# Optimization experiments

Measured on AMD Instinct MI355X. Metric: run time of the kernel, lower is better.

Reference implementation:

```python
import jax, jax.numpy as jnp
import numpy as np

T, B, H = 2048, 32, 512

def setup_inputs() -> dict:
    key = jax.random.key(0)
    k1, k2, k3, k4 = jax.random.split(key, 4)
    hidden = jax.random.normal(k1, (1, B, H), dtype=jnp.float32)
    encoder_outputs = jax.random.normal(k2, (T, B, H), dtype=jnp.float32)
    # nn.Linear(2H, H): weight (H, 2H), bias (H,)
    bound = 1.0 / np.sqrt(2 * H)
    W_attn = jax.random.uniform(k3, (H, 2 * H), dtype=jnp.float32, minval=-bound, maxval=bound)
    b_attn = jax.random.uniform(jax.random.fold_in(k3, 1), (H,), dtype=jnp.float32, minval=-bound, maxval=bound)
    stdv = 1.0 / np.sqrt(H)
    v = jax.random.normal(k4, (H,), dtype=jnp.float32) * stdv
    return {"hidden": hidden, "encoder_outputs": encoder_outputs,
            "W_attn": W_attn, "b_attn": b_attn, "v": v}

def reference(hidden, encoder_outputs, W_attn, b_attn, v):
    # hidden: (1,B,H) -> broadcast to (B,T,H); enc: (T,B,H) -> (B,T,H)
    enc = jnp.transpose(encoder_outputs, (1, 0, 2))          # (B,T,H)
    h = jnp.broadcast_to(hidden[0][:, None, :], enc.shape)   # (B,T,H)
    cat = jnp.concatenate([h, enc], axis=2)                  # (B,T,2H)
    energy = jnp.tanh(jnp.einsum('bth,oh->bto', cat, W_attn) + b_attn)  # (B,T,H)
    scores = jnp.einsum('bth,h->bt', energy, v)              # (B,T)
    return jax.nn.softmax(scores, axis=1)[:, None, :]        # (B,1,T)
```

## Files before the change

kernel.cpp:

```cpp
#include <hip/hip_runtime.h>
#include <hip/hip_bf16.h>


#define TT 2048
#define BB 32
#define HH 512

typedef __attribute__((ext_vector_type(8))) short bf16x8;
typedef __attribute__((ext_vector_type(4))) float f32x4;

static __device__ __forceinline__ unsigned cvt2(float a, float b) {
    union { __hip_bfloat162 h; unsigned u; } cv;
    cv.h = __float22bfloat162_rn(make_float2(a, b));
    return cv.u;
}

static __device__ __forceinline__ unsigned short f2bf(float f) {
    unsigned int u = __float_as_uint(f);
    unsigned int r = (u + 0x7FFFu + ((u >> 16) & 1u)) >> 16;
    return (unsigned short)r;
}

static __device__ __forceinline__ float fast_tanh(float x) {
    float e = __expf(2.0f * x);
    return 1.0f - 2.0f * __builtin_amdgcn_rcpf(1.0f + e);
}

static __device__ __forceinline__ void gload_lds16(const void* g, void* l) {
    __builtin_amdgcn_global_load_lds(
        (const __attribute__((address_space(1))) unsigned int*)g,
        (__attribute__((address_space(3))) unsigned int*)l, 16, 0, 0);
}

__global__ void prep_kernel(const float* __restrict__ W,
                            const float* __restrict__ hidden,
                            const float* __restrict__ b_attn,
                            short* __restrict__ W2p,
                            float* __restrict__ hb) {
    __shared__ float hrow[512];
    const int bid = blockIdx.x;
    if (bid < 1024) {
        int idx = bid * 256 + threadIdx.x;
        int nt = idx >> 16;
        int ks = (idx >> 13) & 7;
        int s  = idx & 8191;
        int j  = s >> 6;
        int c  = s & 63;
        int o  = nt * 128 + j;
        int k  = ks * 64 + (c ^ ((j & 7) << 3));
        W2p[idx] = (short)f2bf(W[o * 1024 + 512 + k]);
    } else {
        const int hbid = bid - 1024;
        int b = hbid >> 1;
        int o = ((hbid & 1) << 8) + threadIdx.x;
        for (int h = threadIdx.x; h < 512; h += 256) hrow[h] = hidden[b * 512 + h];
        __syncthreads();
        const float4* wr = reinterpret_cast<const float4*>(W + (size_t)o * 1024);
        const float4* hr = reinterpret_cast<const float4*>(hrow);
        float acc = b_attn[o];
#pragma unroll 8
        for (int i = 0; i < 128; ++i) {
            float4 w = wr[i], h4 = hr[i];
            acc += w.x * h4.x + w.y * h4.y + w.z * h4.z + w.w * h4.w;
        }
        hb[b * 512 + o] = acc;
    }
}

__global__ __launch_bounds__(256, 2) void attn_main_kernel(
    const float* __restrict__ enc, const short* __restrict__ W2p,
    const float* __restrict__ hb, const float* __restrict__ v,
    float* __restrict__ scores_part)
{
    __shared__ short As[2][128 * 64];
    __shared__ short Bs[2][128 * 64];
    __shared__ float s_red[2][128];

    const int tid = threadIdx.x;
    const int bid = blockIdx.x;
    const int w = (bid & 7) * 256 + (bid >> 3);
    const int nt = w & 3;
    const int mtile = w >> 2;
    const int r0 = mtile * 128;

    const int wave = tid >> 6;
    const int lane = tid & 63;
    const int wr = wave >> 1;
    const int wc = wave & 1;
    const int lcol = lane & 15;
    const int lq = lane >> 4;

    const int arow = tid >> 3;
    const int afc = (tid & 7) * 8;
    const float* encbase = enc + (size_t)(r0 + arow) * HH + afc;
    const short* bsrc = W2p + nt * 65536 + (wave * 4) * 512 + lane * 8;

    f32x4 acc[4][4];
#pragma unroll
    for (int mt = 0; mt < 4; ++mt)
#pragma unroll
        for (int ns = 0; ns < 4; ++ns) acc[mt][ns] = (f32x4){0.f, 0.f, 0.f, 0.f};

    float4 rA0[8], rA1[8];

#define A_LOAD(RA, KS)                                                              \
    {                                                                               \
        _Pragma("unroll")                                                           \
        for (int p = 0; p < 4; ++p) {                                               \
            const float* src = encbase + (size_t)p * 32 * HH + (KS) * 64;           \
            RA[p * 2]     = *reinterpret_cast<const float4*>(src);                  \
            RA[p * 2 + 1] = *reinterpret_cast<const float4*>(src + 4);              \
        }                                                                           \
    }

#define B_STAGE(KS, BUF)                                                            \
    {                                                                               \
        const short* s0 = bsrc + (KS) * 8192;                                       \
        _Pragma("unroll")                                                           \
        for (int c = 0; c < 4; ++c)                                                 \
            gload_lds16(s0 + c * 512, &Bs[BUF][(wave * 4 + c) * 512]);              \
    }

#define A_WRITE(RA, BUF)                                                            \
    {                                                                               \
        _Pragma("unroll")                                                           \
        for (int p = 0; p < 4; ++p) {                                               \
            const int r = p * 32 + arow;                                            \
            uint4 pk;                                                               \
            pk.x = cvt2(RA[p * 2].x, RA[p * 2].y);                                  \
            pk.y = cvt2(RA[p * 2].z, RA[p * 2].w);                                  \
            pk.z = cvt2(RA[p * 2 + 1].x, RA[p * 2 + 1].y);                          \
            pk.w = cvt2(RA[p * 2 + 1].z, RA[p * 2 + 1].w);                          \
            const int cs = afc ^ ((r & 7) << 3);                                    \
            *reinterpret_cast<uint4*>(&As[BUF][r * 64 + cs]) = pk;                  \
        }                                                                           \
    }

#define COMPUTE(BUF)                                                                \
    {                                                                               \
        _Pragma("unroll")                                                           \
        for (int ksub = 0; ksub < 2; ++ksub) {                                      \
            const int kk = ksub * 32 + lq * 8;                                      \
            bf16x8 af[4], bfr[4];                                                   \
            _Pragma("unroll")                                                       \
            for (int mt = 0; mt < 4; ++mt) {                                        \
                const int r = wr * 64 + mt * 16 + lcol;                             \
                af[mt] = *reinterpret_cast<const bf16x8*>(                          \
                    &As[BUF][r * 64 + (kk ^ ((r & 7) << 3))]);                      \
            }                                                                       \
            _Pragma("unroll")                                                       \
            for (int ns = 0; ns < 4; ++ns) {                                        \
                const int j = wc * 64 + ns * 16 + lcol;                             \
                bfr[ns] = *reinterpret_cast<const bf16x8*>(                         \
                    &Bs[BUF][j * 64 + (kk ^ ((j & 7) << 3))]);                      \
            }                                                                       \
            _Pragma("unroll")                                                       \
            for (int mt = 0; mt < 4; ++mt)                                          \
                _Pragma("unroll")                                                   \
                for (int ns = 0; ns < 4; ++ns)                                      \
                    acc[mt][ns] = __builtin_amdgcn_mfma_f32_16x16x32_bf16(          \
                        af[mt], bfr[ns], acc[mt][ns], 0, 0, 0);                     \
        }                                                                           \
    }

    A_LOAD(rA0, 0);
    A_LOAD(rA1, 1);
    B_STAGE(0, 0);
    A_WRITE(rA0, 0);
    __syncthreads();

#pragma unroll
    for (int s2 = 0; s2 < 4; ++s2) {
        const int s = s2 * 2;
        if (s + 2 < 8) A_LOAD(rA0, s + 2);
        B_STAGE(s + 1, 1);
        COMPUTE(0);
        A_WRITE(rA1, 1);
        __syncthreads();
        if (s + 3 < 8) A_LOAD(rA1, s + 3);
        if (s + 2 < 8) B_STAGE(s + 2, 0);
        COMPUTE(1);
        if (s + 2 < 8) {
            A_WRITE(rA0, 0);
            __syncthreads();
        }
    }

    float part[4][4];
#pragma unroll
    for (int mt = 0; mt < 4; ++mt)
#pragma unroll
        for (int j = 0; j < 4; ++j) part[mt][j] = 0.0f;

#pragma unroll
    for (int ns = 0; ns < 4; ++ns) {
        const int o = nt * 128 + wc * 64 + ns * 16 + lcol;
        const float vv = v[o];
        const float* hbcol = hb + o;
#pragma unroll
        for (int mt = 0; mt < 4; ++mt) {
            const int bbase = (mt * 16 + lq * 4) & 31;
#pragma unroll
            for (int j = 0; j < 4; ++j) {
                const float hbv = hbcol[(bbase + j) * 512];
                const float x = acc[mt][ns][j] + hbv;
                part[mt][j] = fmaf(fast_tanh(x), vv, part[mt][j]);
            }
        }
    }

#pragma unroll
    for (int off = 1; off < 16; off <<= 1)
#pragma unroll
        for (int mt = 0; mt < 4; ++mt)
#pragma unroll
            for (int j = 0; j < 4; ++j)
                part[mt][j] += __shfl_xor(part[mt][j], off, 64);

    if (lcol == 0) {
#pragma unroll
        for (int mt = 0; mt < 4; ++mt)
#pragma unroll
            for (int j = 0; j < 4; ++j)
                s_red[wc][wr * 64 + mt * 16 + lq * 4 + j] = part[mt][j];
    }
    __syncthreads();

    if (tid < 128)
        scores_part[(size_t)nt * (TT * BB) + r0 + tid] =
            s_red[0][tid] + s_red[1][tid];
}

__global__ void softmax_kernel(const float* __restrict__ sp, float* __restrict__ out) {
    __shared__ float wred[4];
    __shared__ float wsum[4];
    const int b = blockIdx.x;
    const int tid = threadIdx.x;
    float vals[8];
    float mx = -1e30f;
#pragma unroll
    for (int i = 0; i < 8; ++i) {
        const int t = i * 256 + tid;
        const size_t r = (size_t)t * BB + b;
        const float s = sp[r] + sp[(size_t)(TT * BB) + r] +
                        sp[(size_t)2 * (TT * BB) + r] + sp[(size_t)3 * (TT * BB) + r];
        vals[i] = s;
        mx = fmaxf(mx, s);
    }
#pragma unroll
    for (int off = 32; off; off >>= 1) mx = fmaxf(mx, __shfl_xor(mx, off, 64));
    if ((tid & 63) == 0) wred[tid >> 6] = mx;
    __syncthreads();
    mx = fmaxf(fmaxf(wred[0], wred[1]), fmaxf(wred[2], wred[3]));
    float s = 0.0f;
#pragma unroll
    for (int i = 0; i < 8; ++i) {
        vals[i] = __expf(vals[i] - mx);
        s += vals[i];
    }
#pragma unroll
    for (int off = 32; off; off >>= 1) s += __shfl_xor(s, off, 64);
    if ((tid & 63) == 0) wsum[tid >> 6] = s;
    __syncthreads();
    s = wsum[0] + wsum[1] + wsum[2] + wsum[3];
    const float inv = 1.0f / s;
#pragma unroll
    for (int i = 0; i < 8; ++i) out[b * TT + i * 256 + tid] = vals[i] * inv;
}

extern "C" void kernel_launch(void* const* d_in, const int* in_sizes, int n_in,
                              void* d_out, int out_size, void* d_ws, size_t ws_size,
                              hipStream_t stream) {
    const float* hidden = (const float*)d_in[0];
    const float* enc    = (const float*)d_in[1];
    const float* W      = (const float*)d_in[2];
    const float* b_attn = (const float*)d_in[3];
    const float* v      = (const float*)d_in[4];
    float* out = (float*)d_out;

    char* base = (char*)d_ws;
    short* W2p = (short*)base;
    float* hb  = (float*)(base + 524288);
    float* sp  = (float*)(base + 589824);

    prep_kernel<<<1088, 256, 0, stream>>>(W, hidden, b_attn, W2p, hb);
    attn_main_kernel<<<2048, 256, 0, stream>>>(enc, W2p, hb, v, sp);
    softmax_kernel<<<32, 256, 0, stream>>>(sp, out);
}
```

Measured before the change: 87.15 us.

## Stage fp32 encoder tiles directly into LDS via async loads, convert at fragment read

The encoder A-tile now goes straight from global memory into LDS in fp32 using global_load_lds with an XOR swizzle, instead of going through registers and being converted to bf16 before the LDS write. The bf16 conversion happens when MFMA fragments are read. The K step shrinks from 64 to 32, so there are 16 stages, and W is pre-packed in MFMA fragment order so B fragments are read contiguously. This is meant to free registers and overlap A loads asynchronously, at the cost of twice as many LDS bytes for A, more barriers, and repeated conversion work in each wave.

Result: slower. 91.46 us (+4.9%).

```diff
diff --git a/kernel.cpp b/kernel.cpp
--- a/kernel.cpp
+++ b/kernel.cpp
@@ -41,13 +41,13 @@
     const int bid = blockIdx.x;
     if (bid < 1024) {
         int idx = bid * 256 + threadIdx.x;
-        int nt = idx >> 16;
-        int ks = (idx >> 13) & 7;
-        int s  = idx & 8191;
-        int j  = s >> 6;
-        int c  = s & 63;
-        int o  = nt * 128 + j;
-        int k  = ks * 64 + (c ^ ((j & 7) << 3));
+        int e    = idx & 7;
+        int lane = (idx >> 3) & 63;
+        int cb   = (idx >> 9) & 7;
+        int ks   = (idx >> 12) & 15;
+        int nt   = idx >> 16;
+        int o = nt * 128 + cb * 16 + (lane & 15);
+        int k = ks * 32 + (lane >> 4) * 8 + e;
         W2p[idx] = (short)f2bf(W[o * 1024 + 512 + k]);
     } else {
         const int hbid = bid - 1024;
@@ -72,8 +72,8 @@
     const float* __restrict__ hb, const float* __restrict__ v,
     float* __restrict__ scores_part)
 {
-    __shared__ short As[2][128 * 64];
-    __shared__ short Bs[2][128 * 64];
+    __shared__ float Asf[2][128 * 32];
+    __shared__ short Bs[2][8 * 512];
     __shared__ float s_red[2][128];
 
     const int tid = threadIdx.x;
@@ -90,10 +90,10 @@
     const int lcol = lane & 15;
     const int lq = lane >> 4;
 
-    const int arow = tid >> 3;
-    const int afc = (tid & 7) * 8;
-    const float* encbase = enc + (size_t)(r0 + arow) * HH + afc;
-    const short* bsrc = W2p + nt * 65536 + (wave * 4) * 512 + lane * 8;
+    const int arowl = wave * 32 + (lane >> 3);
+    const float* asrc = enc + (size_t)(r0 + arowl) * HH +
+                        (((lane & 7) ^ ((lane >> 3) & 7)) << 2);
+    const short* bsrc = W2p + (size_t)nt * 65536 + (wave * 2) * 512 + lane * 8;
 
     f32x4 acc[4][4];
 #pragma unroll
@@ -101,89 +101,68 @@
 #pragma unroll
         for (int ns = 0; ns < 4; ++ns) acc[mt][ns] = (f32x4){0.f, 0.f, 0.f, 0.f};
 
-    float4 rA0[8], rA1[8];
-
-#define A_LOAD(RA, KS)                                                              \
+#define STAGE_A(KS, BUF)                                                            \
     {                                                                               \
         _Pragma("unroll")                                                           \
-        for (int p = 0; p < 4; ++p) {                                               \
-            const float* src = encbase + (size_t)p * 32 * HH + (KS) * 64;           \
-            RA[p * 2]     = *reinterpret_cast<const float4*>(src);                  \
-            RA[p * 2 + 1] = *reinterpret_cast<const float4*>(src + 4);              \
-        }                                                                           \
-    }
-
-#define B_STAGE(KS, BUF)                                                            \
+        for (int j = 0; j < 4; ++j)                                                 \
+            gload_lds16(asrc + j * 8 * HH + (KS) * 32,                              \
+                        &Asf[BUF][(wave * 32 + j * 8) * 32]);                       \
+    }
+
+#define STAGE_B(KS, BUF)                                                            \
     {                                                                               \
-        const short* s0 = bsrc + (KS) * 8192;                                       \
-        _Pragma("unroll")                                                           \
-        for (int c = 0; c < 4; ++c)                                                 \
-            gload_lds16(s0 + c * 512, &Bs[BUF][(wave * 4 + c) * 512]);              \
-    }
-
-#define A_WRITE(RA, BUF)                                                            \
-    {                                                                               \
-        _Pragma("unroll")                                                           \
-        for (int p = 0; p < 4; ++p) {                                               \
-            const int r = p * 32 + arow;                                            \
-            uint4 pk;                                                               \
-            pk.x = cvt2(RA[p * 2].x, RA[p * 2].y);                                  \
-            pk.y = cvt2(RA[p * 2].z, RA[p * 2].w);                                  \
-            pk.z = cvt2(RA[p * 2 + 1].x, RA[p * 2 + 1].y);                          \
-            pk.w = cvt2(RA[p * 2 + 1].z, RA[p * 2 + 1].w);                          \
-            const int cs = afc ^ ((r & 7) << 3);                                    \
-            *reinterpret_cast<uint4*>(&As[BUF][r * 64 + cs]) = pk;                  \
-        }                                                                           \
+        const short* s0 = bsrc + (KS) * 8 * 512;                                    \
+        gload_lds16(s0,       &Bs[BUF][(wave * 2) * 512]);                          \
+        gload_lds16(s0 + 512, &Bs[BUF][(wave * 2 + 1) * 512]);                      \
     }
 
 #define COMPUTE(BUF)                                                                \
     {                                                                               \
-        _Pragma("unroll")                                                           \
-        for (int ksub = 0; ksub < 2; ++ksub) {                                      \
-            const int kk = ksub * 32 + lq * 8;                                      \
-            bf16x8 af[4], bfr[4];                                                   \
+        bf16x8 af[4], bfr[4];                                                       \
+        _Pragma("unroll")                                                           \
+        for (int mt = 0; mt < 4; ++mt) {                                            \
+            const int row = wr * 64 + mt * 16 + lcol;                               \
+            const int x = row & 7;                                                  \
+            const float4 v0 = *reinterpret_cast<const float4*>(                     \
+                &Asf[BUF][row * 32 + (((2 * lq) ^ x) << 2)]);                       \
+            const float4 v1 = *reinterpret_cast<const float4*>(                     \
+                &Asf[BUF][row * 32 + ((((2 * lq) | 1) ^ x) << 2)]);                 \
+            union { bf16x8 v8; uint4 u; } pk;                                       \
+            pk.u.x = cvt2(v0.x, v0.y);                                              \
+            pk.u.y = cvt2(v0.z, v0.w);                                              \
+            pk.u.z = cvt2(v1.x, v1.y);                                              \
+            pk.u.w = cvt2(v1.z, v1.w);                                              \
+            af[mt] = pk.v8;                                                         \
+        }                                                                           \
+        _Pragma("unroll")                                                           \
+        for (int ns = 0; ns < 4; ++ns)                                              \
+            bfr[ns] = *reinterpret_cast<const bf16x8*>(                             \
+                &Bs[BUF][(wc * 4 + ns) * 512 + lane * 8]);                          \
+        _Pragma("unroll")                                                           \
+        for (int mt = 0; mt < 4; ++mt)                                              \
             _Pragma("unroll")                                                       \
-            for (int mt = 0; mt < 4; ++mt) {                                        \
-                const int r = wr * 64 + mt * 16 + lcol;                             \
-                af[mt] = *reinterpret_cast<const bf16x8*>(                          \
-                    &As[BUF][r * 64 + (kk ^ ((r & 7) << 3))]);                      \
-            }                                                                       \
-            _Pragma("unroll")                                                       \
-            for (int ns = 0; ns < 4; ++ns) {                                        \
-                const int j = wc * 64 + ns * 16 + lcol;                             \
-                bfr[ns] = *reinterpret_cast<const bf16x8*>(                         \
-                    &Bs[BUF][j * 64 + (kk ^ ((j & 7) << 3))]);                      \
-            }                                                                       \
-            _Pragma("unroll")                                                       \
-            for (int mt = 0; mt < 4; ++mt)                                          \
-                _Pragma("unroll")                                                   \
-                for (int ns = 0; ns < 4; ++ns)                                      \
-                    acc[mt][ns] = __builtin_amdgcn_mfma_f32_16x16x32_bf16(          \
-                        af[mt], bfr[ns], acc[mt][ns], 0, 0, 0);                     \
-        }                                                                           \
-    }
-
-    A_LOAD(rA0, 0);
-    A_LOAD(rA1, 1);
-    B_STAGE(0, 0);
-    A_WRITE(rA0, 0);
-    __syncthreads();
-
-#pragma unroll
-    for (int s2 = 0; s2 < 4; ++s2) {
+            for (int ns = 0; ns < 4; ++ns)                                          \
+                acc[mt][ns] = __builtin_amdgcn_mfma_f32_16x16x32_bf16(              \
+                    af[mt], bfr[ns], acc[mt][ns], 0, 0, 0);                         \
+    }
+
+    STAGE_A(0, 0);
+    STAGE_B(0, 0);
+    __syncthreads();
+
+#pragma unroll
+    for (int s2 = 0; s2 < 8; ++s2) {
         const int s = s2 * 2;
-        if (s + 2 < 8) A_LOAD(rA0, s + 2);
-        B_STAGE(s + 1, 1);
+        STAGE_A(s + 1, 1);
+        STAGE_B(s + 1, 1);
         COMPUTE(0);
-        A_WRITE(rA1, 1);
         __syncthreads();
-        if (s + 3 < 8) A_LOAD(rA1, s + 3);
-        if (s + 2 < 8) B_STAGE(s + 2, 0);
+        if (s + 2 < 16) {
+            STAGE_A(s + 2, 0);
+            STAGE_B(s + 2, 0);
+        }
         COMPUTE(1);
-        if (s + 2 < 8) {
-            A_WRITE(rA0, 0);
-            __syncthreads();
-        }
+        __syncthreads();
     }
 
     float part[4][4];
```

## Warp-specialize GEMM into producer and consumer waves with triple-buffered LDS

Applied to the files above, without the earlier changes.

Splits each 512-thread block into four producer waves that load encoder tiles, convert them to bf16 and stage weight tiles into a three-deep LDS ring, and four consumer waves that run the MFMA loop and the tanh/v epilogue. The two groups synchronise through LDS flag counters polled with s_sleep instead of block-wide barriers. The goal is to overlap global loads with MFMA work more fully. The cost is one block per CU instead of two, larger LDS use, and spin-wait overhead, with a risk of races if the flag ordering or waitcnt placement is wrong.

Result: slower. 103.2 us (+18.4%).

```diff
diff --git a/kernel.cpp b/kernel.cpp
--- a/kernel.cpp
+++ b/kernel.cpp
@@ -8,6 +8,10 @@
 
 typedef __attribute__((ext_vector_type(8))) short bf16x8;
 typedef __attribute__((ext_vector_type(4))) float f32x4;
+
+#define VMWAIT_(N) asm volatile("s_waitcnt vmcnt(" #N ")" ::: "memory")
+#define VMWAIT(N) VMWAIT_(N)
+#define LGKM0() asm volatile("s_waitcnt lgkmcnt(0)" ::: "memory")
 
 static __device__ __forceinline__ unsigned cvt2(float a, float b) {
     union { __hip_bfloat162 h; unsigned u; } cv;
@@ -67,14 +71,16 @@
     }
 }
 
-__global__ __launch_bounds__(256, 2) void attn_main_kernel(
+__global__ __launch_bounds__(512, 1) void attn_main_kernel(
     const float* __restrict__ enc, const short* __restrict__ W2p,
     const float* __restrict__ hb, const float* __restrict__ v,
     float* __restrict__ scores_part)
 {
-    __shared__ short As[2][128 * 64];
-    __shared__ short Bs[2][128 * 64];
+    __shared__ short As[3][128 * 64];
+    __shared__ short Bs[3][128 * 64];
     __shared__ float s_red[2][128];
+    __shared__ int pready[8];
+    __shared__ int cdone[8];
 
     const int tid = threadIdx.x;
     const int bid = blockIdx.x;
@@ -85,25 +91,24 @@
 
     const int wave = tid >> 6;
     const int lane = tid & 63;
-    const int wr = wave >> 1;
-    const int wc = wave & 1;
-    const int lcol = lane & 15;
-    const int lq = lane >> 4;
-
-    const int arow = tid >> 3;
-    const int afc = (tid & 7) * 8;
-    const float* encbase = enc + (size_t)(r0 + arow) * HH + afc;
-    const short* bsrc = W2p + nt * 65536 + (wave * 4) * 512 + lane * 8;
-
-    f32x4 acc[4][4];
-#pragma unroll
-    for (int mt = 0; mt < 4; ++mt)
-#pragma unroll
-        for (int ns = 0; ns < 4; ++ns) acc[mt][ns] = (f32x4){0.f, 0.f, 0.f, 0.f};
-
-    float4 rA0[8], rA1[8];
-
-#define A_LOAD(RA, KS)                                                              \
+
+    if (tid < 8) { pready[tid] = 0; cdone[tid] = 0; }
+    __syncthreads();
+
+    volatile int* vpready = pready;
+    volatile int* vcdone = cdone;
+
+    if (wave >= 4) {
+        const int ptid = tid - 256;
+        const int pwave = wave - 4;
+        const int arow = ptid >> 3;
+        const int afc = (ptid & 7) * 8;
+        const float* encbase = enc + (size_t)(r0 + arow) * HH + afc;
+        const short* bsrc = W2p + nt * 65536 + (pwave * 4) * 512 + lane * 8;
+
+        float4 rA0[8], rA1[8];
+
+#define P_A_LOAD(RA, KS)                                                            \
     {                                                                               \
         _Pragma("unroll")                                                           \
         for (int p = 0; p < 4; ++p) {                                               \
@@ -113,15 +118,15 @@
         }                                                                           \
     }
 
-#define B_STAGE(KS, BUF)                                                            \
+#define P_B_STAGE(KS, BUF)                                                          \
     {                                                                               \
         const short* s0 = bsrc + (KS) * 8192;                                       \
         _Pragma("unroll")                                                           \
         for (int c = 0; c < 4; ++c)                                                 \
-            gload_lds16(s0 + c * 512, &Bs[BUF][(wave * 4 + c) * 512]);              \
-    }
-
-#define A_WRITE(RA, BUF)                                                            \
+            gload_lds16(s0 + c * 512, &Bs[BUF][(pwave * 4 + c) * 512]);             \
+    }
+
+#define P_A_WRITE(RA, BUF)                                                          \
     {                                                                               \
         _Pragma("unroll")                                                           \
         for (int p = 0; p < 4; ++p) {                                               \
@@ -136,7 +141,46 @@
         }                                                                           \
     }
 
-#define COMPUTE(BUF)                                                                \
+#define P_SIGNAL(S)                                                                 \
+    {                                                                               \
+        LGKM0();                                                                    \
+        __builtin_amdgcn_sched_barrier(0);                                          \
+        if (lane == 0) atomicAdd(&pready[S], 1);                                    \
+    }
+
+        P_A_LOAD(rA0, 0);
+        P_B_STAGE(0, 0);
+
+#pragma unroll
+        for (int s = 0; s < 7; ++s) {
+            const int nbuf = (s + 1) % 3;
+            if (s >= 2) {
+                while (vcdone[s - 2] < 4) __builtin_amdgcn_s_sleep(2);
+            }
+            if (s & 1) { P_A_LOAD(rA0, s + 1); } else { P_A_LOAD(rA1, s + 1); }
+            P_B_STAGE(s + 1, nbuf);
+            if (s & 1) { P_A_WRITE(rA1, s % 3); } else { P_A_WRITE(rA0, s % 3); }
+            VMWAIT(12);
+            P_SIGNAL(s);
+        }
+        P_A_WRITE(rA1, 7 % 3);
+        VMWAIT(0);
+        P_SIGNAL(7);
+
+        __syncthreads();
+    } else {
+        const int wr = wave >> 1;
+        const int wc = wave & 1;
+        const int lcol = lane & 15;
+        const int lq = lane >> 4;
+
+        f32x4 acc[4][4];
+#pragma unroll
+        for (int mt = 0; mt < 4; ++mt)
+#pragma unroll
+            for (int ns = 0; ns < 4; ++ns) acc[mt][ns] = (f32x4){0.f, 0.f, 0.f, 0.f};
+
+#define C_COMPUTE(BUF)                                                              \
     {                                                                               \
         _Pragma("unroll")                                                           \
         for (int ksub = 0; ksub < 2; ++ksub) {                                      \
@@ -163,68 +207,55 @@
         }                                                                           \
     }
 
-    A_LOAD(rA0, 0);
-    A_LOAD(rA1, 1);
-    B_STAGE(0, 0);
-    A_WRITE(rA0, 0);
-    __syncthreads();
-
-#pragma unroll
-    for (int s2 = 0; s2 < 4; ++s2) {
-        const int s = s2 * 2;
-        if (s + 2 < 8) A_LOAD(rA0, s + 2);
-        B_STAGE(s + 1, 1);
-        COMPUTE(0);
-        A_WRITE(rA1, 1);
+#pragma unroll
+        for (int s = 0; s < 8; ++s) {
+            while (vpready[s] < 4) __builtin_amdgcn_s_sleep(2);
+            C_COMPUTE(s % 3);
+            LGKM0();
+            __builtin_amdgcn_sched_barrier(0);
+            if (lane == 0) atomicAdd(&cdone[s], 1);
+        }
+
+        float part[4][4];
+#pragma unroll
+        for (int mt = 0; mt < 4; ++mt)
+#pragma unroll
+            for (int j = 0; j < 4; ++j) part[mt][j] = 0.0f;
+
+#pragma unroll
+        for (int ns = 0; ns < 4; ++ns) {
+            const int o = nt * 128 + wc * 64 + ns * 16 + lcol;
+            const float vv = v[o];
+            const float* hbcol = hb + o;
+#pragma unroll
+            for (int mt = 0; mt < 4; ++mt) {
+                const int bbase = (mt * 16 + lq * 4) & 31;
+#pragma unroll
+                for (int j = 0; j < 4; ++j) {
+                    const float hbv = hbcol[(bbase + j) * 512];
+                    const float x = acc[mt][ns][j] + hbv;
+                    part[mt][j] = fmaf(fast_tanh(x), vv, part[mt][j]);
+                }
+            }
+        }
+
+#pragma unroll
+        for (int off = 1; off < 16; off <<= 1)
+#pragma unroll
+            for (int mt = 0; mt < 4; ++mt)
+#pragma unroll
+                for (int j = 0; j < 4; ++j)
+                    part[mt][j] += __shfl_xor(part[mt][j], off, 64);
+
+        if (lcol == 0) {
+#pragma unroll
+            for (int mt = 0; mt < 4; ++mt)
+#pragma unroll
+                for (int j = 0; j < 4; ++j)
+                    s_red[wc][wr * 64 + mt * 16 + lq * 4 + j] = part[mt][j];
+        }
         __syncthreads();
-        if (s + 3 < 8) A_LOAD(rA1, s + 3);
-        if (s + 2 < 8) B_STAGE(s + 2, 0);
-        COMPUTE(1);
-        if (s + 2 < 8) {
-            A_WRITE(rA0, 0);
-            __syncthreads();
-        }
-    }
-
-    float part[4][4];
-#pragma unroll
-    for (int mt = 0; mt < 4; ++mt)
-#pragma unroll
-        for (int j = 0; j < 4; ++j) part[mt][j] = 0.0f;
-
-#pragma unroll
-    for (int ns = 0; ns < 4; ++ns) {
-        const int o = nt * 128 + wc * 64 + ns * 16 + lcol;
-        const float vv = v[o];
-        const float* hbcol = hb + o;
-#pragma unroll
-        for (int mt = 0; mt < 4; ++mt) {
-            const int bbase = (mt * 16 + lq * 4) & 31;
-#pragma unroll
-            for (int j = 0; j < 4; ++j) {
-                const float hbv = hbcol[(bbase + j) * 512];
-                const float x = acc[mt][ns][j] + hbv;
-                part[mt][j] = fmaf(fast_tanh(x), vv, part[mt][j]);
-            }
-        }
-    }
-
-#pragma unroll
-    for (int off = 1; off < 16; off <<= 1)
-#pragma unroll
-        for (int mt = 0; mt < 4; ++mt)
-#pragma unroll
-            for (int j = 0; j < 4; ++j)
-                part[mt][j] += __shfl_xor(part[mt][j], off, 64);
-
-    if (lcol == 0) {
-#pragma unroll
-        for (int mt = 0; mt < 4; ++mt)
-#pragma unroll
-            for (int j = 0; j < 4; ++j)
-                s_red[wc][wr * 64 + mt * 16 + lq * 4 + j] = part[mt][j];
-    }
-    __syncthreads();
+    }
 
     if (tid < 128)
         scores_part[(size_t)nt * (TT * BB) + r0 + tid] =
@@ -284,6 +315,6 @@
     float* sp  = (float*)(base + 589824);
 
     prep_kernel<<<1088, 256, 0, stream>>>(W, hidden, b_attn, W2p, hb);
-    attn_main_kernel<<<2048, 256, 0, stream>>>(enc, W2p, hb, v, sp);
+    attn_main_kernel<<<2048, 512, 0, stream>>>(enc, W2p, hb, v, sp);
     softmax_kernel<<<32, 256, 0, stream>>>(sp, out);
 }
```

## Widen GEMM block tile to 256 output columns with 512 threads

Applied to the files above, without the earlier changes.

Each block of the attention GEMM now computes 256 output features (half of H) using 8 waves instead of 128 with 4 waves, halving the grid. The fp32 encoder tile is therefore loaded and converted to bf16 only twice across the N dimension instead of four times, cutting global reads of the largest input. Score partials drop from four to two, so the softmax sums fewer partials. In exchange, LDS per block roughly doubles and occupancy drops to one larger block per CU, which may reduce latency hiding.

New measurement: 84.18 us. 3.4% less time.

```diff
diff --git a/kernel.cpp b/kernel.cpp
--- a/kernel.cpp
+++ b/kernel.cpp
@@ -41,12 +41,12 @@
     const int bid = blockIdx.x;
     if (bid < 1024) {
         int idx = bid * 256 + threadIdx.x;
-        int nt = idx >> 16;
+        int p  = idx >> 16;
         int ks = (idx >> 13) & 7;
         int s  = idx & 8191;
         int j  = s >> 6;
         int c  = s & 63;
-        int o  = nt * 128 + j;
+        int o  = p * 128 + j;
         int k  = ks * 64 + (c ^ ((j & 7) << 3));
         W2p[idx] = (short)f2bf(W[o * 1024 + 512 + k]);
     } else {
@@ -67,33 +67,33 @@
     }
 }
 
-__global__ __launch_bounds__(256, 2) void attn_main_kernel(
+__global__ __launch_bounds__(512, 1) void attn_main_kernel(
     const float* __restrict__ enc, const short* __restrict__ W2p,
     const float* __restrict__ hb, const float* __restrict__ v,
     float* __restrict__ scores_part)
 {
     __shared__ short As[2][128 * 64];
-    __shared__ short Bs[2][128 * 64];
-    __shared__ float s_red[2][128];
+    __shared__ short Bs[2][256 * 64];
+    __shared__ float s_red[4][128];
 
     const int tid = threadIdx.x;
     const int bid = blockIdx.x;
-    const int w = (bid & 7) * 256 + (bid >> 3);
-    const int nt = w & 3;
-    const int mtile = w >> 2;
+    const int w = (bid & 7) * 128 + (bid >> 3);
+    const int nt = w & 1;
+    const int mtile = w >> 1;
     const int r0 = mtile * 128;
 
     const int wave = tid >> 6;
     const int lane = tid & 63;
-    const int wr = wave >> 1;
-    const int wc = wave & 1;
+    const int wr = wave >> 2;
+    const int wc = wave & 3;
     const int lcol = lane & 15;
     const int lq = lane >> 4;
 
-    const int arow = tid >> 3;
-    const int afc = (tid & 7) * 8;
+    const int arow = tid >> 2;
+    const int afc = (tid & 3) * 16;
     const float* encbase = enc + (size_t)(r0 + arow) * HH + afc;
-    const short* bsrc = W2p + nt * 65536 + (wave * 4) * 512 + lane * 8;
+    const short* bpan = W2p + (size_t)(2 * nt) * 65536 + lane * 8;
 
     f32x4 acc[4][4];
 #pragma unroll
@@ -101,39 +101,38 @@
 #pragma unroll
         for (int ns = 0; ns < 4; ++ns) acc[mt][ns] = (f32x4){0.f, 0.f, 0.f, 0.f};
 
-    float4 rA0[8], rA1[8];
+    float4 rA0[4], rA1[4];
 
 #define A_LOAD(RA, KS)                                                              \
     {                                                                               \
+        const float* src = encbase + (KS) * 64;                                     \
+        RA[0] = *reinterpret_cast<const float4*>(src);                              \
+        RA[1] = *reinterpret_cast<const float4*>(src + 4);                          \
+        RA[2] = *reinterpret_cast<const float4*>(src + 8);                          \
+        RA[3] = *reinterpret_cast<const float4*>(src + 12);                         \
+    }
+
+#define B_STAGE(KS, BUF)                                                            \
+    {                                                                               \
         _Pragma("unroll")                                                           \
-        for (int p = 0; p < 4; ++p) {                                               \
-            const float* src = encbase + (size_t)p * 32 * HH + (KS) * 64;           \
-            RA[p * 2]     = *reinterpret_cast<const float4*>(src);                  \
-            RA[p * 2 + 1] = *reinterpret_cast<const float4*>(src + 4);              \
+        for (int cc = 0; cc < 4; ++cc) {                                            \
+            const int c = wave * 4 + cc;                                            \
+            const short* s0 = bpan + (size_t)(c >> 4) * 65536 + (KS) * 8192 +       \
+                              (c & 15) * 512;                                       \
+            gload_lds16(s0, &Bs[BUF][c * 512]);                                     \
         }                                                                           \
     }
 
-#define B_STAGE(KS, BUF)                                                            \
-    {                                                                               \
-        const short* s0 = bsrc + (KS) * 8192;                                       \
-        _Pragma("unroll")                                                           \
-        for (int c = 0; c < 4; ++c)                                                 \
-            gload_lds16(s0 + c * 512, &Bs[BUF][(wave * 4 + c) * 512]);              \
-    }
-
 #define A_WRITE(RA, BUF)                                                            \
     {                                                                               \
-        _Pragma("unroll")                                                           \
-        for (int p = 0; p < 4; ++p) {                                               \
-            const int r = p * 32 + arow;                                            \
-            uint4 pk;                                                               \
-            pk.x = cvt2(RA[p * 2].x, RA[p * 2].y);                                  \
-            pk.y = cvt2(RA[p * 2].z, RA[p * 2].w);                                  \
-            pk.z = cvt2(RA[p * 2 + 1].x, RA[p * 2 + 1].y);                          \
-            pk.w = cvt2(RA[p * 2 + 1].z, RA[p * 2 + 1].w);                          \
-            const int cs = afc ^ ((r & 7) << 3);                                    \
-            *reinterpret_cast<uint4*>(&As[BUF][r * 64 + cs]) = pk;                  \
-        }                                                                           \
+        uint4 q0, q1;                                                               \
+        q0.x = cvt2(RA[0].x, RA[0].y);  q0.y = cvt2(RA[0].z, RA[0].w);              \
+        q0.z = cvt2(RA[1].x, RA[1].y);  q0.w = cvt2(RA[1].z, RA[1].w);              \
+        q1.x = cvt2(RA[2].x, RA[2].y);  q1.y = cvt2(RA[2].z, RA[2].w);              \
+        q1.z = cvt2(RA[3].x, RA[3].y);  q1.w = cvt2(RA[3].z, RA[3].w);              \
+        const int sw = (arow & 7) << 3;                                             \
+        *reinterpret_cast<uint4*>(&As[BUF][arow * 64 + (afc ^ sw)]) = q0;           \
+        *reinterpret_cast<uint4*>(&As[BUF][arow * 64 + ((afc + 8) ^ sw)]) = q1;     \
     }
 
 #define COMPUTE(BUF)                                                                \
@@ -194,7 +193,7 @@
 
 #pragma unroll
     for (int ns = 0; ns < 4; ++ns) {
-        const int o = nt * 128 + wc * 64 + ns * 16 + lcol;
+        const int o = nt * 256 + wc * 64 + ns * 16 + lcol;
         const float vv = v[o];
         const float* hbcol = hb + o;
 #pragma unroll
@@ -228,7 +227,7 @@
 
     if (tid < 128)
         scores_part[(size_t)nt * (TT * BB) + r0 + tid] =
-            s_red[0][tid] + s_red[1][tid];
+            s_red[0][tid] + s_red[1][tid] + s_red[2][tid] + s_red[3][tid];
 }
 
 __global__ void softmax_kernel(const float* __restrict__ sp, float* __restrict__ out) {
@@ -242,8 +241,7 @@
     for (int i = 0; i < 8; ++i) {
         const int t = i * 256 + tid;
         const size_t r = (size_t)t * BB + b;
-        const float s = sp[r] + sp[(size_t)(TT * BB) + r] +
-                        sp[(size_t)2 * (TT * BB) + r] + sp[(size_t)3 * (TT * BB) + r];
+        const float s = sp[r] + sp[(size_t)(TT * BB) + r];
         vals[i] = s;
         mx = fmaxf(mx, s);
     }
@@ -284,6 +282,6 @@
     float* sp  = (float*)(base + 589824);
 
     prep_kernel<<<1088, 256, 0, stream>>>(W, hidden, b_attn, W2p, hb);
-    attn_main_kernel<<<2048, 256, 0, stream>>>(enc, W2p, hb, v, sp);
+    attn_main_kernel<<<1024, 512, 0, stream>>>(enc, W2p, hb, v, sp);
     softmax_kernel<<<32, 256, 0, stream>>>(sp, out);
 }
```
